# Kernel tuning notes

Hardware: AMD Instinct MI355X
Metric: run time of the kernel (lower is better)

The kernel has to match this reference:

```python
import jax, jax.numpy as jnp
import numpy as np
import math

B, T, D = 2, 2048, 1024
H, HD = 16, 64
MAX_LEN = 2048


def _build_rope_sin_cos(max_seq, head_dim):
    inv_freq = 1.0 / 10000 ** (jnp.arange(0, head_dim, 2) / head_dim)
    positions = jnp.arange(max_seq)
    sinusoid_inp = jnp.einsum('i,j->ij', positions.astype(jnp.float32), inv_freq.astype(jnp.float32))
    sin = jnp.repeat(jnp.sin(sinusoid_inp), 2, axis=-1)
    cos = jnp.repeat(jnp.cos(sinusoid_inp), 2, axis=-1)
    return sin, cos


def _rotate_half(x):
    x1 = x[..., ::2]
    x2 = x[..., 1::2]
    return jnp.stack((-x2, x1), axis=-1).reshape(x.shape)


def setup_inputs() -> dict:
    key = jax.random.key(0)
    ks = jax.random.split(key, 6)
    x = jax.random.normal(ks[0], (B, T, D), dtype=jnp.float32)
    # causal boolean mask (B, T, T)
    mask = jnp.broadcast_to(jnp.tril(jnp.ones((T, T), dtype=bool)), (B, T, T))
    s = 1.0 / math.sqrt(D)
    wq = jax.random.normal(ks[1], (D, H, HD), dtype=jnp.float32) * s
    wk = jax.random.normal(ks[2], (D, H, HD), dtype=jnp.float32) * s
    wv = jax.random.normal(ks[3], (D, H, HD), dtype=jnp.float32) * s
    wo = jax.random.normal(ks[4], (H * HD, D), dtype=jnp.float32) * (1.0 / math.sqrt(H * HD))
    return {"x": x, "mask": mask, "wq": wq, "wk": wk, "wv": wv, "wo": wo}


def reference(x, mask, wq, wk, wv, wo):
    Bx, Tx, Dx = x.shape
    # q/k/v projections: DenseGeneral D -> (H, HD)
    q = jnp.einsum('btd,dhe->bthe', x, wq)
    k = jnp.einsum('btd,dhe->bthe', x, wk)
    v = jnp.einsum('btd,dhe->bthe', x, wv)
    sin, cos = _build_rope_sin_cos(MAX_LEN, HD)
    sin_t = sin[:Tx][None, :, None, :]
    cos_t = cos[:Tx][None, :, None, :]
    q = q * cos_t + _rotate_half(q) * sin_t
    k = k * cos_t + _rotate_half(k) * sin_t
    q = jnp.transpose(q, (0, 2, 1, 3))  # (B,H,T,HD)
    k = jnp.transpose(k, (0, 2, 1, 3))
    v = jnp.transpose(v, (0, 2, 1, 3))
    scale = 1.0 / math.sqrt(HD)
    logits = jnp.einsum('bhqd,bhkd->bhqk', q, k) * scale
    mask_f = mask[:, None, :, :].astype(jnp.float32)
    logits = logits + (1.0 - mask_f) * -1e10
    w = jax.nn.softmax(logits, axis=-1)
    attn_out = jnp.einsum('bhqk,bhkd->bhqd', w, v)
    attn_out = jnp.transpose(attn_out, (0, 2, 1, 3)).reshape(Bx, Tx, -1)
    return attn_out @ wo
```

## Files before the change

kernel.cpp:

```cpp
#include <hip/hip_runtime.h>
#include <cstdint>
#include <cstddef>

typedef __bf16 bf16x8 __attribute__((ext_vector_type(8)));
typedef __bf16 bf16x2 __attribute__((ext_vector_type(2)));
typedef float f32x4 __attribute__((ext_vector_type(4)));
typedef float f32x16 __attribute__((ext_vector_type(16)));
typedef unsigned int u32x4 __attribute__((ext_vector_type(4)));
#define UNROLL _Pragma("unroll")

__device__ __forceinline__ unsigned short f2bf(float f) {
  unsigned int x = __builtin_bit_cast(unsigned int, f);
  x += 0x7fffu + ((x >> 16) & 1u);
  return (unsigned short)(x >> 16);
}
__device__ __forceinline__ float bf2f(unsigned short u) {
  return __builtin_bit_cast(float, (unsigned int)u << 16);
}
__device__ __forceinline__ unsigned int cvtpk(float a, float b) {
  bf16x2 t; t[0] = (__bf16)a; t[1] = (__bf16)b;
  return __builtin_bit_cast(unsigned int, t);
}
__device__ __forceinline__ void async16(const void* g, void* l) {
  __builtin_amdgcn_global_load_lds((void __attribute__((address_space(1)))*)g,
                                   (void __attribute__((address_space(3)))*)l,
                                   16, 0, 0);
}

__global__ void prep_x(const float* __restrict__ x, unsigned short* __restrict__ xb) {
  int i = blockIdx.x * 256 + threadIdx.x;
  const float4* p = (const float4*)(x + (size_t)i * 8);
  float4 a = p[0], b = p[1];
  ushort4 o0 = {f2bf(a.x), f2bf(a.y), f2bf(a.z), f2bf(a.w)};
  ushort4 o1 = {f2bf(b.x), f2bf(b.y), f2bf(b.z), f2bf(b.w)};
  ushort4* q = (ushort4*)(xb + (size_t)i * 8);
  q[0] = o0; q[1] = o1;
}

__global__ void prep_w(const float* __restrict__ wq, const float* __restrict__ wk,
                       const float* __restrict__ wv, const float* __restrict__ wo,
                       unsigned short* __restrict__ out) {
  __shared__ float tile[32][33];
  const float* src = blockIdx.z == 0 ? wq : blockIdx.z == 1 ? wk : blockIdx.z == 2 ? wv : wo;
  unsigned short* dst = out + (size_t)blockIdx.z * 1048576;
  int kb = blockIdx.x * 32, nb = blockIdx.y * 32;
  int c = threadIdx.x & 31, r4 = (threadIdx.x >> 5) * 4;
UNROLL
  for (int i = 0; i < 4; ++i)
    tile[r4 + i][c] = src[(size_t)(kb + r4 + i) * 1024 + nb + c];
  __syncthreads();
UNROLL
  for (int i = 0; i < 4; ++i)
    dst[(size_t)(nb + r4 + i) * 1024 + kb + c] = f2bf(tile[c][r4 + i]);
}

__global__ void prep_rope(float2* __restrict__ tab) {
  int idx = blockIdx.x * 256 + threadIdx.x;
  int t = idx >> 5, i = idx & 31;
  float inv = exp2f(-(float)i * (13.287712379549449f / 32.0f));
  float ang = (float)t * inv;
  tab[idx] = make_float2(cosf(ang), sinf(ang));
}

template <int EPI>
__global__ __launch_bounds__(256, 3) void gemm_bt(
    const unsigned short* __restrict__ A, const unsigned short* __restrict__ Bt,
    void* __restrict__ outp, unsigned short* __restrict__ kout,
    unsigned short* __restrict__ vtout, const float2* __restrict__ rope) {
  __shared__ unsigned short As[128 * 32];
  __shared__ unsigned short Bs[128 * 32];
  const int tid = threadIdx.x;
  const int lane = tid & 63, wid = tid >> 6;
  const int wr = wid >> 1, wc = wid & 1;
  const int g = lane >> 4, r16 = lane & 15;
  const int m0 = blockIdx.y * 128, n0 = blockIdx.x * 128;

  f32x4 acc[4][4];
UNROLL
  for (int i = 0; i < 4; ++i)
UNROLL
    for (int j = 0; j < 4; ++j) acc[i][j] = (f32x4){0.f, 0.f, 0.f, 0.f};

  const int arow = tid >> 2;
  const int acol = (tid & 3) * 8;
  const unsigned short* gA = A + (size_t)(m0 + arow) * 1024 + acol;
  const unsigned short* gB = Bt + (size_t)(n0 + arow) * 1024 + acol;
  unsigned short* lA = As + tid * 8;
  unsigned short* lB = Bs + tid * 8;

  for (int k0 = 0; k0 < 1024; k0 += 32) {
    async16(gA + k0, lA);
    async16(gA + k0 + 64 * 1024, lA + 64 * 32);
    async16(gB + k0, lB);
    async16(gB + k0 + 64 * 1024, lB + 64 * 32);
    __syncthreads();
    bf16x8 af[4], bfr[4];
UNROLL
    for (int mi = 0; mi < 4; ++mi)
      af[mi] = *(const bf16x8*)&As[(wr * 64 + mi * 16 + r16) * 32 + g * 8];
UNROLL
    for (int ni = 0; ni < 4; ++ni)
      bfr[ni] = *(const bf16x8*)&Bs[(wc * 64 + ni * 16 + r16) * 32 + g * 8];
UNROLL
    for (int mi = 0; mi < 4; ++mi)
UNROLL
      for (int ni = 0; ni < 4; ++ni)
        acc[mi][ni] = __builtin_amdgcn_mfma_f32_16x16x32_bf16(af[mi], bfr[ni],
                                                              acc[mi][ni], 0, 0, 0);
    __syncthreads();
  }

  if constexpr (EPI == 0) {
    unsigned short* qout = (unsigned short*)outp;
    const int which = n0 >> 10;
    const int b = (m0 >= 2048) ? 1 : 0;
    const float QSCL = 0.18033688011112042f;
UNROLL
    for (int mi = 0; mi < 4; ++mi) {
      const int rowb = m0 + wr * 64 + mi * 16 + g * 4;
      const int trow = rowb & 2047;
UNROLL
      for (int ni = 0; ni < 4; ++ni) {
        const int n = n0 + wc * 64 + ni * 16 + r16;
        const int h = (n >> 6) & 15, e = n & 63;
        f32x4 v = acc[mi][ni];
        if (which < 2) {
          const int fi = e >> 1;
          const bool ev = (e & 1) == 0;
UNROLL
          for (int j = 0; j < 4; ++j) {
            float2 cs = rope[(trow + j) * 32 + fi];
            float p = __shfl_xor(v[j], 1);
            v[j] = ev ? (v[j] * cs.x - p * cs.y) : (v[j] * cs.x + p * cs.y);
          }
          if (which == 0) { v[0] *= QSCL; v[1] *= QSCL; v[2] *= QSCL; v[3] *= QSCL; }
        }
        if (which == 2) {
          size_t base = (((size_t)b * 16 + h) * 64 + e) * 2048 + trow;
          ushort4 pkv = {f2bf(v[0]), f2bf(v[1]), f2bf(v[2]), f2bf(v[3])};
          *(ushort4*)(vtout + base) = pkv;
        } else {
          unsigned short* dst = (which == 0) ? qout : kout;
          size_t base = (((size_t)b * 16 + h) * 2048 + trow) * 64 + e;
UNROLL
          for (int j = 0; j < 4; ++j) dst[base + (size_t)j * 64] = f2bf(v[j]);
        }
      }
    }
  } else {
    float* out = (float*)outp;
UNROLL
    for (int mi = 0; mi < 4; ++mi) {
      const int rowb = m0 + wr * 64 + mi * 16 + g * 4;
UNROLL
      for (int ni = 0; ni < 4; ++ni) {
        const int n = n0 + wc * 64 + ni * 16 + r16;
UNROLL
        for (int j = 0; j < 4; ++j)
          out[(size_t)(rowb + j) * 1024 + n] = acc[mi][ni][j];
      }
    }
  }
}

__device__ const int g_qt[24] = {7,15,15,14,14,6,13,13,12,12,5,11,11,10,10,4,9,9,8,8,3,2,1,0};
__device__ const int g_hf[24] = {-1,0,1,0,1,-1,0,1,0,1,-1,0,1,0,1,-1,0,1,0,1,-1,-1,-1,-1};

__global__ __launch_bounds__(256, 3) void attn3(
    const unsigned short* __restrict__ qb, const unsigned short* __restrict__ kb,
    const unsigned short* __restrict__ vtb, unsigned short* __restrict__ attnb,
    unsigned short* __restrict__ po, float2* __restrict__ ml) {
  __shared__ __align__(16) char smem[2][16384];
  const int tid = threadIdx.x;
  const int lane = tid & 63, w = tid >> 6;
  const int l31 = lane & 31, h = lane >> 5;
  const int bh = blockIdx.x;
  const int qt = g_qt[blockIdx.y];
  const int hf = g_hf[blockIdx.y];
  const int q0b = qt * 128;
  const int q0w = q0b + w * 32;
  const int qg = q0w + l31;
  const size_t kvbase = (size_t)bh * (2048 * 64);
  const int t0 = (hf == 1) ? (qt + 1) : 0;
  const int t1 = (hf == 0) ? (qt + 1) : (2 * qt + 2);

  bf16x8 qf[4];
  const unsigned short* qp = qb + kvbase + (size_t)qg * 64 + h * 8;
UNROLL
  for (int kk = 0; kk < 4; ++kk) qf[kk] = *(const bf16x8*)(qp + kk * 16);

  const int lr = lane >> 3;
  const int cb2 = ((lane & 7) ^ lr) << 3;
  const bool isK = (w < 2);
  const int c0 = isK ? w * 4 : (w - 2) * 4;
  const unsigned short* srcp[4];
  int dstoff[4];
  const size_t step = isK ? 4096 : 64;
UNROLL
  for (int s = 0; s < 4; ++s) {
    int r = (c0 + s) * 8 + lr;
    srcp[s] = isK ? (kb + kvbase + (size_t)r * 64 + cb2)
                  : (vtb + kvbase + (size_t)r * 2048 + cb2);
    dstoff[s] = (w * 4 + s) * 1024 + lane * 16;
  }

  f32x16 o0, o1;
UNROLL
  for (int r = 0; r < 16; ++r) { o0[r] = 0.f; o1[r] = 0.f; }
  float m_run = -3e38f, l_run = 0.f;

UNROLL
  for (int s = 0; s < 4; ++s) async16(srcp[s] + (size_t)t0 * step, &smem[0][0] + dstoff[s]);
  __syncthreads();

  const int swz = (l31 & 7) << 4;
  for (int t = t0; t < t1; ++t) {
    const int kt0 = t << 6;
    if (t + 1 < t1) {
      char* db = &smem[(t + 1 - t0) & 1][0];
UNROLL
      for (int s = 0; s < 4; ++s)
        async16(srcp[s] + (size_t)(t + 1) * step, db + dstoff[s]);
    }
    if (kt0 <= q0w + 31) {
      const char* cbuf = &smem[(t - t0) & 1][0];
      f32x16 sa, sb;
UNROLL
      for (int r = 0; r < 16; ++r) { sa[r] = 0.f; sb[r] = 0.f; }
      __builtin_amdgcn_s_setprio(1);
UNROLL
      for (int kk = 0; kk < 4; ++kk) {
        bf16x8 kf = *(const bf16x8*)(cbuf + l31 * 128 + ((kk * 32 + h * 16) ^ swz));
        sa = __builtin_amdgcn_mfma_f32_32x32x16_bf16(kf, qf[kk], sa, 0, 0, 0);
      }
UNROLL
      for (int kk = 0; kk < 4; ++kk) {
        bf16x8 kf = *(const bf16x8*)(cbuf + (32 + l31) * 128 + ((kk * 32 + h * 16) ^ swz));
        sb = __builtin_amdgcn_mfma_f32_32x32x16_bf16(kf, qf[kk], sb, 0, 0, 0);
      }
      __builtin_amdgcn_s_setprio(0);
      if (kt0 + 63 > q0w) {
UNROLL
        for (int r = 0; r < 16; ++r) {
          int koff = (r & 3) + 8 * (r >> 2) + 4 * h;
          if (kt0 + koff > qg) sa[r] = -3e38f;
          if (kt0 + 32 + koff > qg) sb[r] = -3e38f;
        }
      }
      float cm = -3e38f;
UNROLL
      for (int r = 0; r < 16; ++r) { cm = fmaxf(cm, sa[r]); cm = fmaxf(cm, sb[r]); }
      cm = fmaxf(cm, __shfl_xor(cm, 32));
      if (__any(cm > m_run + 8.f)) {
        float mn = fmaxf(cm, m_run);
        float al = exp2f(m_run - mn);
        l_run *= al;
        o0 *= al; o1 *= al;
        m_run = mn;
      }
      float ps = 0.f;
UNROLL
      for (int r = 0; r < 16; ++r) {
        sa[r] = exp2f(sa[r] - m_run);
        sb[r] = exp2f(sb[r] - m_run);
        ps += sa[r] + sb[r];
      }
      ps += __shfl_xor(ps, 32);
      l_run += ps;
      unsigned int lo[8], hi[8];
UNROLL
      for (int b8 = 0; b8 < 4; ++b8) {
        lo[b8]     = cvtpk(sa[4 * b8], sa[4 * b8 + 1]);
        hi[b8]     = cvtpk(sa[4 * b8 + 2], sa[4 * b8 + 3]);
        lo[4 + b8] = cvtpk(sb[4 * b8], sb[4 * b8 + 1]);
        hi[4 + b8] = cvtpk(sb[4 * b8 + 2], sb[4 * b8 + 3]);
      }
      bf16x8 pa[4];
UNROLL
      for (int j = 0; j < 4; ++j) {
        const int bb = (j >> 1) * 4 + (j & 1) * 2;
        unsigned int a0 = lo[bb], b0 = lo[bb + 1];
        unsigned int a1 = hi[bb], b1 = hi[bb + 1];
        asm volatile("v_permlane32_swap_b32 %0, %1" : "+v"(a0), "+v"(b0));
        asm volatile("v_permlane32_swap_b32 %0, %1" : "+v"(a1), "+v"(b1));
        u32x4 f;
        f[0] = a0; f[1] = a1; f[2] = b0; f[3] = b1;
        pa[j] = __builtin_bit_cast(bf16x8, f);
      }
      __builtin_amdgcn_s_setprio(1);
UNROLL
      for (int j = 0; j < 4; ++j) {
        bf16x8 v0 = *(const bf16x8*)(cbuf + 8192 + l31 * 128 + ((j * 32 + h * 16) ^ swz));
        bf16x8 v1 = *(const bf16x8*)(cbuf + 8192 + (32 + l31) * 128 + ((j * 32 + h * 16) ^ swz));
        o0 = __builtin_amdgcn_mfma_f32_32x32x16_bf16(pa[j], v0, o0, 0, 0, 0);
        o1 = __builtin_amdgcn_mfma_f32_32x32x16_bf16(pa[j], v1, o1, 0, 0, 0);
      }
      __builtin_amdgcn_s_setprio(0);
    }
    __syncthreads();
  }

  float* lsh = (float*)&smem[0][0] + w * 32;
  if (h == 0) lsh[l31] = 1.0f / l_run;
  __syncthreads();
  f32x4 inv[4];
UNROLL
  for (int rg = 0; rg < 4; ++rg) inv[rg] = *(const f32x4*)&lsh[8 * rg + 4 * h];
  if (hf < 0) {
    const int b = bh >> 4, hh = bh & 15;
UNROLL
    for (int r = 0; r < 16; ++r) {
      const int qg2 = q0w + (r & 3) + 8 * (r >> 2) + 4 * h;
      const size_t base = (((size_t)b * 2048 + qg2) * 16 + hh) * 64 + l31;
      const float iv = inv[r >> 2][r & 3];
      attnb[base]      = f2bf(o0[r] * iv);
      attnb[base + 32] = f2bf(o1[r] * iv);
    }
  } else {
    const int p = bh * 16 + (qt - 8) * 2 + hf;
    if (h == 0) ml[p * 128 + w * 32 + l31] = make_float2(m_run, l_run);
    unsigned short* pb = po + (size_t)p * 8192;
UNROLL
    for (int r = 0; r < 16; ++r) {
      const int rl = w * 32 + (r & 3) + 8 * (r >> 2) + 4 * h;
      const float iv = inv[r >> 2][r & 3];
      pb[rl * 64 + l31]      = f2bf(o0[r] * iv);
      pb[rl * 64 + l31 + 32] = f2bf(o1[r] * iv);
    }
  }
}

__global__ void attn_combine(const unsigned short* __restrict__ po,
                             const float2* __restrict__ ml,
                             unsigned short* __restrict__ attnb) {
  const int idx = blockIdx.x * 256 + threadIdx.x;
  const int c8 = idx & 7;
  const int row = (idx >> 3) & 127;
  const int qi = (idx >> 10) & 7;
  const int bh = idx >> 13;
  const int p0 = bh * 16 + qi * 2;
  const float2 e0 = ml[p0 * 128 + row];
  const float2 e1 = ml[(p0 + 1) * 128 + row];
  const float M = fmaxf(e0.x, e1.x);
  float w0 = e0.y * exp2f(e0.x - M);
  float w1 = e1.y * exp2f(e1.x - M);
  const float inv = 1.0f / (w0 + w1);
  w0 *= inv; w1 *= inv;
  const ushort4* a = (const ushort4*)(po + (size_t)p0 * 8192 + row * 64 + c8 * 8);
  const ushort4* b = (const ushort4*)(po + (size_t)(p0 + 1) * 8192 + row * 64 + c8 * 8);
  ushort4 A0 = a[0], A1 = a[1], B0 = b[0], B1 = b[1];
  ushort4 O0, O1;
  O0.x = f2bf(w0 * bf2f(A0.x) + w1 * bf2f(B0.x));
  O0.y = f2bf(w0 * bf2f(A0.y) + w1 * bf2f(B0.y));
  O0.z = f2bf(w0 * bf2f(A0.z) + w1 * bf2f(B0.z));
  O0.w = f2bf(w0 * bf2f(A0.w) + w1 * bf2f(B0.w));
  O1.x = f2bf(w0 * bf2f(A1.x) + w1 * bf2f(B1.x));
  O1.y = f2bf(w0 * bf2f(A1.y) + w1 * bf2f(B1.y));
  O1.z = f2bf(w0 * bf2f(A1.z) + w1 * bf2f(B1.z));
  O1.w = f2bf(w0 * bf2f(A1.w) + w1 * bf2f(B1.w));
  const int bq = bh >> 4, hh = bh & 15;
  const int q = (qi + 8) * 128 + row;
  ushort4* out = (ushort4*)(attnb + (((size_t)bq * 2048 + q) * 16 + hh) * 64 + c8 * 8);
  out[0] = O0; out[1] = O1;
}

extern "C" void kernel_launch(void* const* d_in, const int* in_sizes, int n_in,
                              void* d_out, int out_size, void* d_ws, size_t ws_size,
                              hipStream_t stream) {
  (void)in_sizes; (void)n_in; (void)out_size; (void)ws_size;
  const float* x = (const float*)d_in[0];
  const float* wq = (const float*)d_in[2];
  const float* wk = (const float*)d_in[3];
  const float* wv = (const float*)d_in[4];
  const float* wo = (const float*)d_in[5];

  unsigned short* xb = (unsigned short*)d_ws;
  unsigned short* wT = xb + 4 * 1024 * 1024;
  float2* rope = (float2*)(wT + 4 * 1024 * 1024);
  unsigned short* qb = (unsigned short*)(rope + 65536);
  unsigned short* kbuf = qb + 4 * 1024 * 1024;
  unsigned short* vtb = kbuf + 4 * 1024 * 1024;
  unsigned short* attnb = vtb + 4 * 1024 * 1024;

  unsigned short* po = xb;
  float2* mlb = rope;

  prep_x<<<dim3(2048), dim3(256), 0, stream>>>(x, xb);
  prep_w<<<dim3(32, 32, 4), dim3(256), 0, stream>>>(wq, wk, wv, wo, wT);
  prep_rope<<<dim3(256), dim3(256), 0, stream>>>(rope);
  gemm_bt<0><<<dim3(24, 32), dim3(256), 0, stream>>>(xb, wT, qb, kbuf, vtb, rope);
  attn3<<<dim3(32, 24), dim3(256), 0, stream>>>(qb, kbuf, vtb, attnb, po, mlb);
  attn_combine<<<dim3(1024), dim3(256), 0, stream>>>(po, mlb, attnb);
  gemm_bt<1><<<dim3(8, 32), dim3(256), 0, stream>>>(attnb, wT + 3 * 1024 * 1024,
                                                    d_out, nullptr, nullptr, nullptr);
}
```

Baseline: 121.4 us.

## Replace QKV projection GEMM with 256x256-tile pipelined kernel

```diff
diff --git a/kernel.cpp b/kernel.cpp
--- a/kernel.cpp
+++ b/kernel.cpp
@@ -62,11 +62,131 @@
   tab[idx] = make_float2(cosf(ang), sinf(ang));
 }
 
+__global__ __launch_bounds__(512, 2) void gemm256(
+    const unsigned short* __restrict__ A, const unsigned short* __restrict__ Bt,
+    unsigned short* __restrict__ qout, unsigned short* __restrict__ kout,
+    unsigned short* __restrict__ vtout, const float2* __restrict__ rope) {
+  __shared__ __align__(16) char sm[2][32768];
+  const int tid = threadIdx.x;
+  const int lane = tid & 63, wid = tid >> 6;
+  const int wm = wid >> 2, wn = wid & 3;
+  const int g = lane >> 4, r16 = lane & 15;
+
+  const int wg = (blockIdx.x & 7) * 24 + (blockIdx.x >> 3);
+  const int m0 = (wg & 15) * 256, n0 = (wg >> 4) * 256;
+
+  const int sxor = (r16 & 8) << 2;
+  const int aoffb = (wm * 8192 + r16 * 64 + g * 16) ^ sxor;
+  const int boffb = 16384 + ((wn * 4096 + r16 * 64 + g * 16) ^ sxor);
+
+  const int xorb = ((tid >> 5) & 1) << 5;
+  const unsigned short* srcA[2];
+  const unsigned short* srcB[2];
+  int dsto[2];
+UNROLL
+  for (int sw = 0; sw < 2; ++sw) {
+    const int d = sw * 8192 + tid * 16;
+    const int e = d ^ xorb;
+    const int row = e >> 6, kus = (e & 63) >> 1;
+    srcA[sw] = A + (size_t)(m0 + row) * 1024 + kus;
+    srcB[sw] = Bt + (size_t)(n0 + row) * 1024 + kus;
+    dsto[sw] = d;
+  }
+#define STAGE_A(tt) { char* _d = &sm[(tt) & 1][0]; \
+    async16(srcA[0] + (size_t)(tt) * 32, _d + dsto[0]); \
+    async16(srcA[1] + (size_t)(tt) * 32, _d + dsto[1]); }
+#define STAGE_B(tt) { char* _d = &sm[(tt) & 1][16384]; \
+    async16(srcB[0] + (size_t)(tt) * 32, _d + dsto[0]); \
+    async16(srcB[1] + (size_t)(tt) * 32, _d + dsto[1]); }
+
+  f32x4 acc[8][4];
+UNROLL
+  for (int i = 0; i < 8; ++i)
+UNROLL
+    for (int j = 0; j < 4; ++j) acc[i][j] = (f32x4){0.f, 0.f, 0.f, 0.f};
+
+  STAGE_A(0); STAGE_B(0); STAGE_B(1);
+  asm volatile("s_waitcnt vmcnt(2)" ::: "memory");
+  __builtin_amdgcn_s_barrier();
+
+  for (int t = 0; t < 32; ++t) {
+    const char* cb = &sm[t & 1][0];
+    bf16x8 aq[4], bq[4];
+UNROLL
+    for (int nf = 0; nf < 4; ++nf) bq[nf] = *(const bf16x8*)(cb + boffb + nf * 1024);
+UNROLL
+    for (int mf = 0; mf < 4; ++mf) aq[mf] = *(const bf16x8*)(cb + aoffb + mf * 1024);
+    if (t + 1 < 32) STAGE_A(t + 1);
+    __builtin_amdgcn_s_barrier();
+    __builtin_amdgcn_s_setprio(1);
+UNROLL
+    for (int mf = 0; mf < 4; ++mf)
+UNROLL
+      for (int nf = 0; nf < 4; ++nf)
+        acc[mf][nf] = __builtin_amdgcn_mfma_f32_16x16x32_bf16(aq[mf], bq[nf],
+                                                              acc[mf][nf], 0, 0, 0);
+    __builtin_amdgcn_s_setprio(0);
+    __builtin_amdgcn_s_barrier();
+UNROLL
+    for (int mf = 0; mf < 4; ++mf) aq[mf] = *(const bf16x8*)(cb + aoffb + (mf + 4) * 1024);
+    if (t + 2 < 32) STAGE_B(t + 2);
+    __builtin_amdgcn_s_barrier();
+    __builtin_amdgcn_s_setprio(1);
+UNROLL
+    for (int mf = 0; mf < 4; ++mf)
+UNROLL
+      for (int nf = 0; nf < 4; ++nf)
+        acc[mf + 4][nf] = __builtin_amdgcn_mfma_f32_16x16x32_bf16(aq[mf], bq[nf],
+                                                                  acc[mf + 4][nf], 0, 0, 0);
+    __builtin_amdgcn_s_setprio(0);
+    if (t < 30) { asm volatile("s_waitcnt vmcnt(2)" ::: "memory"); }
+    else        { asm volatile("s_waitcnt vmcnt(0)" ::: "memory"); }
+    __builtin_amdgcn_s_barrier();
+  }
+#undef STAGE_A
+#undef STAGE_B
+
+  const int which = n0 >> 10;
+  const int b = (m0 >= 2048) ? 1 : 0;
+  const float QSCL = 0.18033688011112042f;
+UNROLL
+  for (int mf = 0; mf < 8; ++mf) {
+    const int rowb = m0 + wm * 128 + mf * 16 + g * 4;
+    const int trow = rowb & 2047;
+UNROLL
+    for (int nf = 0; nf < 4; ++nf) {
+      const int n = n0 + wn * 64 + nf * 16 + r16;
+      const int h = (n >> 6) & 15, e = n & 63;
+      f32x4 v = acc[mf][nf];
+      if (which < 2) {
+        const int fi = e >> 1;
+        const bool ev = (e & 1) == 0;
+UNROLL
+        for (int j = 0; j < 4; ++j) {
+          float2 cs = rope[(trow + j) * 32 + fi];
+          float p = __shfl_xor(v[j], 1);
+          v[j] = ev ? (v[j] * cs.x - p * cs.y) : (v[j] * cs.x + p * cs.y);
+        }
+        if (which == 0) { v[0] *= QSCL; v[1] *= QSCL; v[2] *= QSCL; v[3] *= QSCL; }
+      }
+      if (which == 2) {
+        size_t base = (((size_t)b * 16 + h) * 64 + e) * 2048 + trow;
+        ushort4 pkv = {f2bf(v[0]), f2bf(v[1]), f2bf(v[2]), f2bf(v[3])};
+        *(ushort4*)(vtout + base) = pkv;
+      } else {
+        unsigned short* dst = (which == 0) ? qout : kout;
+        size_t base = (((size_t)b * 16 + h) * 2048 + trow) * 64 + e;
+UNROLL
+        for (int j = 0; j < 4; ++j) dst[base + (size_t)j * 64] = f2bf(v[j]);
+      }
+    }
+  }
+}
+
 template <int EPI>
 __global__ __launch_bounds__(256, 3) void gemm_bt(
     const unsigned short* __restrict__ A, const unsigned short* __restrict__ Bt,
-    void* __restrict__ outp, unsigned short* __restrict__ kout,
-    unsigned short* __restrict__ vtout, const float2* __restrict__ rope) {
+    void* __restrict__ outp) {
   __shared__ unsigned short As[128 * 32];
   __shared__ unsigned short Bs[128 * 32];
   const int tid = threadIdx.x;
@@ -110,55 +230,16 @@
     __syncthreads();
   }
 
-  if constexpr (EPI == 0) {
-    unsigned short* qout = (unsigned short*)outp;
-    const int which = n0 >> 10;
-    const int b = (m0 >= 2048) ? 1 : 0;
-    const float QSCL = 0.18033688011112042f;
-UNROLL
-    for (int mi = 0; mi < 4; ++mi) {
-      const int rowb = m0 + wr * 64 + mi * 16 + g * 4;
-      const int trow = rowb & 2047;
-UNROLL
-      for (int ni = 0; ni < 4; ++ni) {
-        const int n = n0 + wc * 64 + ni * 16 + r16;
-        const int h = (n >> 6) & 15, e = n & 63;
-        f32x4 v = acc[mi][ni];
-        if (which < 2) {
-          const int fi = e >> 1;
-          const bool ev = (e & 1) == 0;
-UNROLL
-          for (int j = 0; j < 4; ++j) {
-            float2 cs = rope[(trow + j) * 32 + fi];
-            float p = __shfl_xor(v[j], 1);
-            v[j] = ev ? (v[j] * cs.x - p * cs.y) : (v[j] * cs.x + p * cs.y);
-          }
-          if (which == 0) { v[0] *= QSCL; v[1] *= QSCL; v[2] *= QSCL; v[3] *= QSCL; }
-        }
-        if (which == 2) {
-          size_t base = (((size_t)b * 16 + h) * 64 + e) * 2048 + trow;
-          ushort4 pkv = {f2bf(v[0]), f2bf(v[1]), f2bf(v[2]), f2bf(v[3])};
-          *(ushort4*)(vtout + base) = pkv;
-        } else {
-          unsigned short* dst = (which == 0) ? qout : kout;
-          size_t base = (((size_t)b * 16 + h) * 2048 + trow) * 64 + e;
-UNROLL
-          for (int j = 0; j < 4; ++j) dst[base + (size_t)j * 64] = f2bf(v[j]);
-        }
-      }
-    }
-  } else {
-    float* out = (float*)outp;
-UNROLL
-    for (int mi = 0; mi < 4; ++mi) {
-      const int rowb = m0 + wr * 64 + mi * 16 + g * 4;
-UNROLL
-      for (int ni = 0; ni < 4; ++ni) {
-        const int n = n0 + wc * 64 + ni * 16 + r16;
-UNROLL
-        for (int j = 0; j < 4; ++j)
-          out[(size_t)(rowb + j) * 1024 + n] = acc[mi][ni][j];
-      }
+  float* out = (float*)outp;
+UNROLL
+  for (int mi = 0; mi < 4; ++mi) {
+    const int rowb = m0 + wr * 64 + mi * 16 + g * 4;
+UNROLL
+    for (int ni = 0; ni < 4; ++ni) {
+      const int n = n0 + wc * 64 + ni * 16 + r16;
+UNROLL
+      for (int j = 0; j < 4; ++j)
+        out[(size_t)(rowb + j) * 1024 + n] = acc[mi][ni][j];
     }
   }
 }
@@ -388,9 +469,9 @@
   prep_x<<<dim3(2048), dim3(256), 0, stream>>>(x, xb);
   prep_w<<<dim3(32, 32, 4), dim3(256), 0, stream>>>(wq, wk, wv, wo, wT);
   prep_rope<<<dim3(256), dim3(256), 0, stream>>>(rope);
-  gemm_bt<0><<<dim3(24, 32), dim3(256), 0, stream>>>(xb, wT, qb, kbuf, vtb, rope);
+  gemm256<<<dim3(192), dim3(512), 0, stream>>>(xb, wT, qb, kbuf, vtb, rope);
   attn3<<<dim3(32, 24), dim3(256), 0, stream>>>(qb, kbuf, vtb, attnb, po, mlb);
   attn_combine<<<dim3(1024), dim3(256), 0, stream>>>(po, mlb, attnb);
   gemm_bt<1><<<dim3(8, 32), dim3(256), 0, stream>>>(attnb, wT + 3 * 1024 * 1024,
-                                                    d_out, nullptr, nullptr, nullptr);
-}
+                                                    d_out);
+}
```

Result: no change. 122.4 us (+0.9%).

## Rewrite QKV GEMM with 256x256 double-buffered swizzled tiles; shrink O-proj tiles

Applied to the files above, without the earlier changes.

```diff
diff --git a/kernel.cpp b/kernel.cpp
--- a/kernel.cpp
+++ b/kernel.cpp
@@ -62,27 +62,152 @@
   tab[idx] = make_float2(cosf(ang), sinf(ang));
 }
 
-template <int EPI>
-__global__ __launch_bounds__(256, 3) void gemm_bt(
+__global__ __launch_bounds__(512, 2) void gemmqkv(
     const unsigned short* __restrict__ A, const unsigned short* __restrict__ Bt,
-    void* __restrict__ outp, unsigned short* __restrict__ kout,
+    unsigned short* __restrict__ qout, unsigned short* __restrict__ kout,
     unsigned short* __restrict__ vtout, const float2* __restrict__ rope) {
-  __shared__ unsigned short As[128 * 32];
+  __shared__ __align__(16) char sm[2][65536];
+  const int tid = threadIdx.x;
+  const int lane = tid & 63, wid = tid >> 6;
+  const int wm = wid >> 2, wn = wid & 3;
+  const int g = lane >> 4, r16 = lane & 15;
+
+  const int wg = (blockIdx.x & 7) * 24 + (blockIdx.x >> 3);
+  const int m0 = (wg & 15) * 256, n0 = (wg >> 4) * 256;
+
+  const int swz = (r16 & 7) << 4;
+  const int co0 = (g * 16) ^ swz;
+  const int co1 = (64 + g * 16) ^ swz;
+  const int abase = wm * 16384 + r16 * 128;
+  const int brow0 = wn * 64 + r16;
+
+  const unsigned short* gA = A + (size_t)m0 * 1024;
+  const unsigned short* gB = Bt + (size_t)n0 * 1024;
+  const int srow = tid >> 3;
+  const int ce = ((tid & 7) ^ (srow & 7)) << 3;
+  const int dst0 = tid * 16;
+
+#define STG_A(bb, h, u) { char* _d = &sm[bb][(h) * 16384] + dst0; \
+    async16(gA + (size_t)((h) * 128 + srow) * 1024 + (u) * 64 + ce, _d); \
+    async16(gA + (size_t)((h) * 128 + 64 + srow) * 1024 + (u) * 64 + ce, _d + 8192); }
+#define STG_B(bb, h, u) { char* _d = &sm[bb][32768 + (h) * 16384] + dst0; \
+    async16(gB + (size_t)((h) * 128 + srow) * 1024 + (u) * 64 + ce, _d); \
+    async16(gB + (size_t)((h) * 128 + 64 + srow) * 1024 + (u) * 64 + ce, _d + 8192); }
+#define RD_A(dst, cb, mfb) UNROLL for (int mf = 0; mf < 4; ++mf) { \
+    dst[mf][0] = *(const bf16x8*)((cb) + abase + ((mfb) + mf) * 2048 + co0); \
+    dst[mf][1] = *(const bf16x8*)((cb) + abase + ((mfb) + mf) * 2048 + co1); }
+#define RD_B(dst, cb, nfb) UNROLL for (int nf = 0; nf < 2; ++nf) { \
+    const int br = brow0 + ((nfb) + nf) * 16; \
+    const int bo = 32768 + ((br >> 7) << 14) + (br & 127) * 128; \
+    dst[nf][0] = *(const bf16x8*)((cb) + bo + co0); \
+    dst[nf][1] = *(const bf16x8*)((cb) + bo + co1); }
+#define MM(mfb, afr, bfr, nfb) \
+    __builtin_amdgcn_s_setprio(1); \
+    UNROLL for (int mf = 0; mf < 4; ++mf) \
+    UNROLL for (int nf = 0; nf < 2; ++nf) \
+    UNROLL for (int kk = 0; kk < 2; ++kk) \
+      acc[(mfb) + mf][(nfb) + nf] = __builtin_amdgcn_mfma_f32_16x16x32_bf16( \
+          afr[mf][kk], bfr[nf][kk], acc[(mfb) + mf][(nfb) + nf], 0, 0, 0); \
+    __builtin_amdgcn_s_setprio(0);
+
+  f32x4 acc[8][4];
+UNROLL
+  for (int i = 0; i < 8; ++i)
+UNROLL
+    for (int j = 0; j < 4; ++j) acc[i][j] = (f32x4){0.f, 0.f, 0.f, 0.f};
+
+  bf16x8 alo[4][2], ahi[4][2], blo[2][2], bhi[2][2];
+
+  STG_A(0, 0, 0) STG_A(0, 1, 0) STG_B(0, 0, 0) STG_B(0, 1, 0)
+  STG_A(1, 0, 1) STG_A(1, 1, 1)
+  asm volatile("s_waitcnt vmcnt(4)" ::: "memory");
+  __builtin_amdgcn_s_barrier();
+
+  for (int u = 0; u < 16; ++u) {
+    const int bsel = u & 1;
+    const char* cb = &sm[bsel][0];
+    RD_A(alo, cb, 0)
+    RD_B(blo, cb, 0)
+    if (u + 1 < 16) STG_B(bsel ^ 1, 0, u + 1)
+    __builtin_amdgcn_s_barrier();
+    MM(0, alo, blo, 0)
+    __builtin_amdgcn_s_barrier();
+    RD_A(ahi, cb, 4)
+    if (u + 1 < 16) STG_B(bsel ^ 1, 1, u + 1)
+    __builtin_amdgcn_s_barrier();
+    MM(4, ahi, blo, 0)
+    __builtin_amdgcn_s_barrier();
+    RD_B(bhi, cb, 2)
+    if (u + 2 < 16) { STG_A(bsel, 0, u + 2) STG_A(bsel, 1, u + 2) }
+    __builtin_amdgcn_s_barrier();
+    MM(4, ahi, bhi, 2)
+    __builtin_amdgcn_s_barrier();
+    MM(0, alo, bhi, 2)
+    if (u < 14) { asm volatile("s_waitcnt vmcnt(4)" ::: "memory"); }
+    else        { asm volatile("s_waitcnt vmcnt(0)" ::: "memory"); }
+    __builtin_amdgcn_s_barrier();
+  }
+#undef STG_A
+#undef STG_B
+#undef RD_A
+#undef RD_B
+#undef MM
+
+  const int which = n0 >> 10;
+  const int b = (m0 >= 2048) ? 1 : 0;
+  const float QSCL = 0.18033688011112042f;
+UNROLL
+  for (int mf = 0; mf < 8; ++mf) {
+    const int rowb = m0 + wm * 128 + mf * 16 + g * 4;
+    const int trow = rowb & 2047;
+UNROLL
+    for (int nf = 0; nf < 4; ++nf) {
+      const int n = n0 + wn * 64 + nf * 16 + r16;
+      const int h = (n >> 6) & 15, e = n & 63;
+      f32x4 v = acc[mf][nf];
+      if (which < 2) {
+        const int fi = e >> 1;
+        const bool ev = (e & 1) == 0;
+UNROLL
+        for (int j = 0; j < 4; ++j) {
+          float2 cs = rope[(trow + j) * 32 + fi];
+          float p = __shfl_xor(v[j], 1);
+          v[j] = ev ? (v[j] * cs.x - p * cs.y) : (v[j] * cs.x + p * cs.y);
+        }
+        if (which == 0) { v[0] *= QSCL; v[1] *= QSCL; v[2] *= QSCL; v[3] *= QSCL; }
+      }
+      if (which == 2) {
+        size_t base = (((size_t)b * 16 + h) * 64 + e) * 2048 + trow;
+        ushort4 pkv = {f2bf(v[0]), f2bf(v[1]), f2bf(v[2]), f2bf(v[3])};
+        *(ushort4*)(vtout + base) = pkv;
+      } else {
+        unsigned short* dst = (which == 0) ? qout : kout;
+        size_t base = (((size_t)b * 16 + h) * 2048 + trow) * 64 + e;
+UNROLL
+        for (int j = 0; j < 4; ++j) dst[base + (size_t)j * 64] = f2bf(v[j]);
+      }
+    }
+  }
+}
+
+__global__ __launch_bounds__(256, 3) void gemm_o(
+    const unsigned short* __restrict__ A, const unsigned short* __restrict__ Bt,
+    float* __restrict__ out) {
+  __shared__ unsigned short As[64 * 32];
   __shared__ unsigned short Bs[128 * 32];
   const int tid = threadIdx.x;
   const int lane = tid & 63, wid = tid >> 6;
-  const int wr = wid >> 1, wc = wid & 1;
+  const int wm = wid >> 1, wn = wid & 1;
   const int g = lane >> 4, r16 = lane & 15;
-  const int m0 = blockIdx.y * 128, n0 = blockIdx.x * 128;
-
-  f32x4 acc[4][4];
-UNROLL
-  for (int i = 0; i < 4; ++i)
+  const int m0 = blockIdx.y * 64, n0 = blockIdx.x * 128;
+
+  f32x4 acc[2][4];
+UNROLL
+  for (int i = 0; i < 2; ++i)
 UNROLL
     for (int j = 0; j < 4; ++j) acc[i][j] = (f32x4){0.f, 0.f, 0.f, 0.f};
 
-  const int arow = tid >> 2;
-  const int acol = (tid & 3) * 8;
+  const int arow = tid >> 2, acol = (tid & 3) * 8;
   const unsigned short* gA = A + (size_t)(m0 + arow) * 1024 + acol;
   const unsigned short* gB = Bt + (size_t)(n0 + arow) * 1024 + acol;
   unsigned short* lA = As + tid * 8;
@@ -90,19 +215,18 @@
 
   for (int k0 = 0; k0 < 1024; k0 += 32) {
     async16(gA + k0, lA);
-    async16(gA + k0 + 64 * 1024, lA + 64 * 32);
     async16(gB + k0, lB);
     async16(gB + k0 + 64 * 1024, lB + 64 * 32);
     __syncthreads();
-    bf16x8 af[4], bfr[4];
-UNROLL
-    for (int mi = 0; mi < 4; ++mi)
-      af[mi] = *(const bf16x8*)&As[(wr * 64 + mi * 16 + r16) * 32 + g * 8];
+    bf16x8 af[2], bfr[4];
+UNROLL
+    for (int mi = 0; mi < 2; ++mi)
+      af[mi] = *(const bf16x8*)&As[(wm * 32 + mi * 16 + r16) * 32 + g * 8];
 UNROLL
     for (int ni = 0; ni < 4; ++ni)
-      bfr[ni] = *(const bf16x8*)&Bs[(wc * 64 + ni * 16 + r16) * 32 + g * 8];
-UNROLL
-    for (int mi = 0; mi < 4; ++mi)
+      bfr[ni] = *(const bf16x8*)&Bs[(wn * 64 + ni * 16 + r16) * 32 + g * 8];
+UNROLL
+    for (int mi = 0; mi < 2; ++mi)
 UNROLL
       for (int ni = 0; ni < 4; ++ni)
         acc[mi][ni] = __builtin_amdgcn_mfma_f32_16x16x32_bf16(af[mi], bfr[ni],
@@ -110,55 +234,15 @@
     __syncthreads();
   }
 
-  if constexpr (EPI == 0) {
-    unsigned short* qout = (unsigned short*)outp;
-    const int which = n0 >> 10;
-    const int b = (m0 >= 2048) ? 1 : 0;
-    const float QSCL = 0.18033688011112042f;
-UNROLL
-    for (int mi = 0; mi < 4; ++mi) {
-      const int rowb = m0 + wr * 64 + mi * 16 + g * 4;
-      const int trow = rowb & 2047;
-UNROLL
-      for (int ni = 0; ni < 4; ++ni) {
-        const int n = n0 + wc * 64 + ni * 16 + r16;
-        const int h = (n >> 6) & 15, e = n & 63;
-        f32x4 v = acc[mi][ni];
-        if (which < 2) {
-          const int fi = e >> 1;
-          const bool ev = (e & 1) == 0;
-UNROLL
-          for (int j = 0; j < 4; ++j) {
-            float2 cs = rope[(trow + j) * 32 + fi];
-            float p = __shfl_xor(v[j], 1);
-            v[j] = ev ? (v[j] * cs.x - p * cs.y) : (v[j] * cs.x + p * cs.y);
-          }
-          if (which == 0) { v[0] *= QSCL; v[1] *= QSCL; v[2] *= QSCL; v[3] *= QSCL; }
-        }
-        if (which == 2) {
-          size_t base = (((size_t)b * 16 + h) * 64 + e) * 2048 + trow;
-          ushort4 pkv = {f2bf(v[0]), f2bf(v[1]), f2bf(v[2]), f2bf(v[3])};
-          *(ushort4*)(vtout + base) = pkv;
-        } else {
-          unsigned short* dst = (which == 0) ? qout : kout;
-          size_t base = (((size_t)b * 16 + h) * 2048 + trow) * 64 + e;
-UNROLL
-          for (int j = 0; j < 4; ++j) dst[base + (size_t)j * 64] = f2bf(v[j]);
-        }
-      }
-    }
-  } else {
-    float* out = (float*)outp;
-UNROLL
-    for (int mi = 0; mi < 4; ++mi) {
-      const int rowb = m0 + wr * 64 + mi * 16 + g * 4;
-UNROLL
-      for (int ni = 0; ni < 4; ++ni) {
-        const int n = n0 + wc * 64 + ni * 16 + r16;
-UNROLL
-        for (int j = 0; j < 4; ++j)
-          out[(size_t)(rowb + j) * 1024 + n] = acc[mi][ni][j];
-      }
+UNROLL
+  for (int mi = 0; mi < 2; ++mi) {
+    const int rowb = m0 + wm * 32 + mi * 16 + g * 4;
+UNROLL
+    for (int ni = 0; ni < 4; ++ni) {
+      const int n = n0 + wn * 64 + ni * 16 + r16;
+UNROLL
+      for (int j = 0; j < 4; ++j)
+        out[(size_t)(rowb + j) * 1024 + n] = acc[mi][ni][j];
     }
   }
 }
@@ -388,9 +472,9 @@
   prep_x<<<dim3(2048), dim3(256), 0, stream>>>(x, xb);
   prep_w<<<dim3(32, 32, 4), dim3(256), 0, stream>>>(wq, wk, wv, wo, wT);
   prep_rope<<<dim3(256), dim3(256), 0, stream>>>(rope);
-  gemm_bt<0><<<dim3(24, 32), dim3(256), 0, stream>>>(xb, wT, qb, kbuf, vtb, rope);
+  gemmqkv<<<dim3(192), dim3(512), 0, stream>>>(xb, wT, qb, kbuf, vtb, rope);
   attn3<<<dim3(32, 24), dim3(256), 0, stream>>>(qb, kbuf, vtb, attnb, po, mlb);
   attn_combine<<<dim3(1024), dim3(256), 0, stream>>>(po, mlb, attnb);
-  gemm_bt<1><<<dim3(8, 32), dim3(256), 0, stream>>>(attnb, wT + 3 * 1024 * 1024,
-                                                    d_out, nullptr, nullptr, nullptr);
-}
+  gemm_o<<<dim3(8, 64), dim3(256), 0, stream>>>(attnb, wT + 3 * 1024 * 1024,
+                                                (float*)d_out);
+}
```

Result: faster. 116.9 us (-3.7%).

## Double K-tile depth with XOR-swizzled LDS and split output GEMM into smaller tiles

Applied to the files above, without the earlier changes.

```diff
diff --git a/kernel.cpp b/kernel.cpp
--- a/kernel.cpp
+++ b/kernel.cpp
@@ -62,13 +62,12 @@
   tab[idx] = make_float2(cosf(ang), sinf(ang));
 }
 
-template <int EPI>
-__global__ __launch_bounds__(256, 3) void gemm_bt(
+__global__ __launch_bounds__(256, 3) void gemmqkv(
     const unsigned short* __restrict__ A, const unsigned short* __restrict__ Bt,
-    void* __restrict__ outp, unsigned short* __restrict__ kout,
+    unsigned short* __restrict__ qout, unsigned short* __restrict__ kout,
     unsigned short* __restrict__ vtout, const float2* __restrict__ rope) {
-  __shared__ unsigned short As[128 * 32];
-  __shared__ unsigned short Bs[128 * 32];
+  __shared__ __align__(16) unsigned short As[128 * 64];
+  __shared__ __align__(16) unsigned short Bs[128 * 64];
   const int tid = threadIdx.x;
   const int lane = tid & 63, wid = tid >> 6;
   const int wr = wid >> 1, wc = wid & 1;
@@ -81,84 +80,142 @@
 UNROLL
     for (int j = 0; j < 4; ++j) acc[i][j] = (f32x4){0.f, 0.f, 0.f, 0.f};
 
-  const int arow = tid >> 2;
-  const int acol = (tid & 3) * 8;
-  const unsigned short* gA = A + (size_t)(m0 + arow) * 1024 + acol;
-  const unsigned short* gB = Bt + (size_t)(n0 + arow) * 1024 + acol;
-  unsigned short* lA = As + tid * 8;
-  unsigned short* lB = Bs + tid * 8;
-
-  for (int k0 = 0; k0 < 1024; k0 += 32) {
-    async16(gA + k0, lA);
-    async16(gA + k0 + 64 * 1024, lA + 64 * 32);
-    async16(gB + k0, lB);
-    async16(gB + k0 + 64 * 1024, lB + 64 * 32);
+  const int ce = (((tid & 7) ^ ((tid >> 3) & 7)) << 3);
+  const unsigned short* gA = A + (size_t)(m0 + (tid >> 3)) * 1024 + ce;
+  const unsigned short* gB = Bt + (size_t)(n0 + (tid >> 3)) * 1024 + ce;
+  char* lA = (char*)As + tid * 16;
+  char* lB = (char*)Bs + tid * 16;
+
+  const int swz = (r16 & 7) << 4;
+
+  for (int u = 0; u < 16; ++u) {
+    const int k0 = u * 64;
+UNROLL
+    for (int s = 0; s < 4; ++s) {
+      async16(gA + (size_t)s * 32 * 1024 + k0, lA + s * 4096);
+      async16(gB + (size_t)s * 32 * 1024 + k0, lB + s * 4096);
+    }
     __syncthreads();
-    bf16x8 af[4], bfr[4];
-UNROLL
-    for (int mi = 0; mi < 4; ++mi)
-      af[mi] = *(const bf16x8*)&As[(wr * 64 + mi * 16 + r16) * 32 + g * 8];
-UNROLL
-    for (int ni = 0; ni < 4; ++ni)
-      bfr[ni] = *(const bf16x8*)&Bs[(wc * 64 + ni * 16 + r16) * 32 + g * 8];
-UNROLL
-    for (int mi = 0; mi < 4; ++mi)
+UNROLL
+    for (int kk = 0; kk < 2; ++kk) {
+      bf16x8 af[4], bfr[4];
+UNROLL
+      for (int mi = 0; mi < 4; ++mi)
+        af[mi] = *(const bf16x8*)((const char*)As +
+                  (wr * 64 + mi * 16 + r16) * 128 + ((kk * 64 + g * 16) ^ swz));
 UNROLL
       for (int ni = 0; ni < 4; ++ni)
-        acc[mi][ni] = __builtin_amdgcn_mfma_f32_16x16x32_bf16(af[mi], bfr[ni],
-                                                              acc[mi][ni], 0, 0, 0);
+        bfr[ni] = *(const bf16x8*)((const char*)Bs +
+                  (wc * 64 + ni * 16 + r16) * 128 + ((kk * 64 + g * 16) ^ swz));
+UNROLL
+      for (int mi = 0; mi < 4; ++mi)
+UNROLL
+        for (int ni = 0; ni < 4; ++ni)
+          acc[mi][ni] = __builtin_amdgcn_mfma_f32_16x16x32_bf16(af[mi], bfr[ni],
+                                                                acc[mi][ni], 0, 0, 0);
+    }
     __syncthreads();
   }
 
-  if constexpr (EPI == 0) {
-    unsigned short* qout = (unsigned short*)outp;
-    const int which = n0 >> 10;
-    const int b = (m0 >= 2048) ? 1 : 0;
-    const float QSCL = 0.18033688011112042f;
-UNROLL
-    for (int mi = 0; mi < 4; ++mi) {
-      const int rowb = m0 + wr * 64 + mi * 16 + g * 4;
-      const int trow = rowb & 2047;
-UNROLL
-      for (int ni = 0; ni < 4; ++ni) {
-        const int n = n0 + wc * 64 + ni * 16 + r16;
-        const int h = (n >> 6) & 15, e = n & 63;
-        f32x4 v = acc[mi][ni];
-        if (which < 2) {
-          const int fi = e >> 1;
-          const bool ev = (e & 1) == 0;
-UNROLL
-          for (int j = 0; j < 4; ++j) {
-            float2 cs = rope[(trow + j) * 32 + fi];
-            float p = __shfl_xor(v[j], 1);
-            v[j] = ev ? (v[j] * cs.x - p * cs.y) : (v[j] * cs.x + p * cs.y);
-          }
-          if (which == 0) { v[0] *= QSCL; v[1] *= QSCL; v[2] *= QSCL; v[3] *= QSCL; }
+  const int which = n0 >> 10;
+  const int b = (m0 >= 2048) ? 1 : 0;
+  const float QSCL = 0.18033688011112042f;
+UNROLL
+  for (int mi = 0; mi < 4; ++mi) {
+    const int rowb = m0 + wr * 64 + mi * 16 + g * 4;
+    const int trow = rowb & 2047;
+UNROLL
+    for (int ni = 0; ni < 4; ++ni) {
+      const int n = n0 + wc * 64 + ni * 16 + r16;
+      const int h = (n >> 6) & 15, e = n & 63;
+      f32x4 v = acc[mi][ni];
+      if (which < 2) {
+        const int fi = e >> 1;
+        const bool ev = (e & 1) == 0;
+UNROLL
+        for (int j = 0; j < 4; ++j) {
+          float2 cs = rope[(trow + j) * 32 + fi];
+          float p = __shfl_xor(v[j], 1);
+          v[j] = ev ? (v[j] * cs.x - p * cs.y) : (v[j] * cs.x + p * cs.y);
         }
-        if (which == 2) {
-          size_t base = (((size_t)b * 16 + h) * 64 + e) * 2048 + trow;
-          ushort4 pkv = {f2bf(v[0]), f2bf(v[1]), f2bf(v[2]), f2bf(v[3])};
-          *(ushort4*)(vtout + base) = pkv;
-        } else {
-          unsigned short* dst = (which == 0) ? qout : kout;
-          size_t base = (((size_t)b * 16 + h) * 2048 + trow) * 64 + e;
-UNROLL
-          for (int j = 0; j < 4; ++j) dst[base + (size_t)j * 64] = f2bf(v[j]);
-        }
-      }
-    }
-  } else {
-    float* out = (float*)outp;
-UNROLL
-    for (int mi = 0; mi < 4; ++mi) {
-      const int rowb = m0 + wr * 64 + mi * 16 + g * 4;
-UNROLL
-      for (int ni = 0; ni < 4; ++ni) {
-        const int n = n0 + wc * 64 + ni * 16 + r16;
-UNROLL
-        for (int j = 0; j < 4; ++j)
-          out[(size_t)(rowb + j) * 1024 + n] = acc[mi][ni][j];
-      }
+        if (which == 0) { v[0] *= QSCL; v[1] *= QSCL; v[2] *= QSCL; v[3] *= QSCL; }
+      }
+      if (which == 2) {
+        size_t base = (((size_t)b * 16 + h) * 64 + e) * 2048 + trow;
+        ushort4 pkv = {f2bf(v[0]), f2bf(v[1]), f2bf(v[2]), f2bf(v[3])};
+        *(ushort4*)(vtout + base) = pkv;
+      } else {
+        unsigned short* dst = (which == 0) ? qout : kout;
+        size_t base = (((size_t)b * 16 + h) * 2048 + trow) * 64 + e;
+UNROLL
+        for (int j = 0; j < 4; ++j) dst[base + (size_t)j * 64] = f2bf(v[j]);
+      }
+    }
+  }
+}
+
+__global__ __launch_bounds__(256, 4) void gemm_o(
+    const unsigned short* __restrict__ A, const unsigned short* __restrict__ Bt,
+    float* __restrict__ out) {
+  __shared__ __align__(16) unsigned short As[64 * 64];
+  __shared__ __align__(16) unsigned short Bs[64 * 64];
+  const int tid = threadIdx.x;
+  const int lane = tid & 63, wid = tid >> 6;
+  const int wm = wid >> 1, wn = wid & 1;
+  const int g = lane >> 4, r16 = lane & 15;
+  const int m0 = blockIdx.y * 64, n0 = blockIdx.x * 64;
+
+  f32x4 acc[2][2];
+UNROLL
+  for (int i = 0; i < 2; ++i)
+UNROLL
+    for (int j = 0; j < 2; ++j) acc[i][j] = (f32x4){0.f, 0.f, 0.f, 0.f};
+
+  const int ce = (((tid & 7) ^ ((tid >> 3) & 7)) << 3);
+  const unsigned short* gA = A + (size_t)(m0 + (tid >> 3)) * 1024 + ce;
+  const unsigned short* gB = Bt + (size_t)(n0 + (tid >> 3)) * 1024 + ce;
+  char* lA = (char*)As + tid * 16;
+  char* lB = (char*)Bs + tid * 16;
+  const int swz = (r16 & 7) << 4;
+
+  for (int u = 0; u < 16; ++u) {
+    const int k0 = u * 64;
+UNROLL
+    for (int s = 0; s < 2; ++s) {
+      async16(gA + (size_t)s * 32 * 1024 + k0, lA + s * 4096);
+      async16(gB + (size_t)s * 32 * 1024 + k0, lB + s * 4096);
+    }
+    __syncthreads();
+UNROLL
+    for (int kk = 0; kk < 2; ++kk) {
+      bf16x8 af[2], bfr[2];
+UNROLL
+      for (int mi = 0; mi < 2; ++mi)
+        af[mi] = *(const bf16x8*)((const char*)As +
+                  (wm * 32 + mi * 16 + r16) * 128 + ((kk * 64 + g * 16) ^ swz));
+UNROLL
+      for (int ni = 0; ni < 2; ++ni)
+        bfr[ni] = *(const bf16x8*)((const char*)Bs +
+                  (wn * 32 + ni * 16 + r16) * 128 + ((kk * 64 + g * 16) ^ swz));
+UNROLL
+      for (int mi = 0; mi < 2; ++mi)
+UNROLL
+        for (int ni = 0; ni < 2; ++ni)
+          acc[mi][ni] = __builtin_amdgcn_mfma_f32_16x16x32_bf16(af[mi], bfr[ni],
+                                                                acc[mi][ni], 0, 0, 0);
+    }
+    __syncthreads();
+  }
+
+UNROLL
+  for (int mi = 0; mi < 2; ++mi) {
+    const int rowb = m0 + wm * 32 + mi * 16 + g * 4;
+UNROLL
+    for (int ni = 0; ni < 2; ++ni) {
+      const int n = n0 + wn * 32 + ni * 16 + r16;
+UNROLL
+      for (int j = 0; j < 4; ++j)
+        out[(size_t)(rowb + j) * 1024 + n] = acc[mi][ni][j];
     }
   }
 }
@@ -388,9 +445,9 @@
   prep_x<<<dim3(2048), dim3(256), 0, stream>>>(x, xb);
   prep_w<<<dim3(32, 32, 4), dim3(256), 0, stream>>>(wq, wk, wv, wo, wT);
   prep_rope<<<dim3(256), dim3(256), 0, stream>>>(rope);
-  gemm_bt<0><<<dim3(24, 32), dim3(256), 0, stream>>>(xb, wT, qb, kbuf, vtb, rope);
+  gemmqkv<<<dim3(24, 32), dim3(256), 0, stream>>>(xb, wT, qb, kbuf, vtb, rope);
   attn3<<<dim3(32, 24), dim3(256), 0, stream>>>(qb, kbuf, vtb, attnb, po, mlb);
   attn_combine<<<dim3(1024), dim3(256), 0, stream>>>(po, mlb, attnb);
-  gemm_bt<1><<<dim3(8, 32), dim3(256), 0, stream>>>(attnb, wT + 3 * 1024 * 1024,
-                                                    d_out, nullptr, nullptr, nullptr);
-}
+  gemm_o<<<dim3(16, 64), dim3(256), 0, stream>>>(attnb, wT + 3 * 1024 * 1024,
+                                                 (float*)d_out);
+}
```

Result: faster. 112.8 us (-7.1%).
